# Performance work log

Measured on AMD Instinct MI355X. Metric: run time of the kernel, lower is better.

Reference implementation:

```python
import jax, jax.numpy as jnp
import numpy as np
from jax import lax

DN = ('NDHWC', 'DHWIO', 'NDHWC')
SHAPE = (33, 33, 33)
B = 2
N = 40000
C = 64


def setup_inputs() -> dict:
    key = jax.random.key(0)
    ks = jax.random.split(key, 24)
    D, H, W = SHAPE
    # unique active voxel coords (batch, z, y, x)
    rng = np.random.default_rng(0)
    idx = rng.choice(B * D * H * W, size=N, replace=False)
    b = idx // (D * H * W)
    r = idx % (D * H * W)
    coors = np.stack([b, r // (H * W), (r // W) % H, r % W], axis=1).astype(np.int32)

    def w(k, shape, scale=0.1):
        return jax.random.normal(k, shape, jnp.float32) * scale

    inp = {
        'features': jax.random.normal(ks[0], (N, 3), jnp.float32),
        'coors': jnp.asarray(coors),
        'batch_size': B,
        'w1': w(ks[1], (3, 3, 3, 3, C), 0.2), 'b1': w(ks[2], (C,), 0.05),
        'w2': w(ks[3], (3, 3, 3, C, C), 0.05), 'b2': w(ks[4], (C,), 0.05),
        'w3': w(ks[5], (3, 3, 3, C, C), 0.05), 'b3': w(ks[6], (C,), 0.05),
        'wt': w(ks[7], (3, 3, 3, C, C), 0.05), 'bt': w(ks[8], (C,), 0.05),
        'w5': w(ks[9], (3, 3, 3, C, C), 0.05), 'b5': w(ks[10], (C,), 0.05),
    }
    # folded eval-mode BatchNorm: y = x*s + h  (s = gamma/sqrt(var+eps), h = beta - mean*s)
    for i, (sk, hk) in enumerate(zip(ks[11:16], ks[16:21]), start=1):
        inp[f's{i}'] = 1.0 + 0.1 * jax.random.normal(sk, (C,), jnp.float32)
        inp[f'h{i}'] = 0.05 * jax.random.normal(hk, (C,), jnp.float32)
    return inp


def _forward(features, coors, batch_size,
             w1, b1, w2, b2, w3, b3, wt, bt, w5, b5,
             s1, h1, s2, h2, s3, h3, s4, h4, s5, h5):
    D, H, W = SHAPE
    bi, zi, yi, xi = coors[:, 0], coors[:, 1], coors[:, 2], coors[:, 3]
    # densify SparseConvTensor (zeros at inactive sites) + active mask
    x = jnp.zeros((batch_size, D, H, W, features.shape[-1]), features.dtype)
    x = x.at[bi, zi, yi, xi].set(features)
    m = jnp.zeros((batch_size, D, H, W, 1), jnp.float32).at[bi, zi, yi, xi].set(1.0)
    ones3 = jnp.ones((3, 3, 3, 1, 1), jnp.float32)

    conv = lambda a, k, pad: lax.conv_general_dilated(a, k, (1, 1, 1), pad, dimension_numbers=DN)
    # masked BN(eval) + ReLU: applied only on active sites, background stays exactly 0
    act = lambda y, mm, s, h: jnp.where(mm, jax.nn.relu(y * s + h), 0.0)

    # SparseConv3d(3,64,3): valid conv; output actives = 1-dilation of input actives
    x = conv(x, w1, 'VALID')
    m1 = conv(m, ones3, 'VALID') > 0  # [B,31,31,31,1]
    x = act(x + b1, m1, s1, h1)

    # two SubMConv3d(64,64,3) sharing indice_key: same active set, SAME padding
    x = act(conv(x, w2, 'SAME') + b2, m1, s2, h2)
    x = act(conv(x, w3, 'SAME') + b3, m1, s3, h3)

    # SparseConvTranspose3d(64,64,3,2): out = (D-1)*2+3; actives = transposed dilation
    x = lax.conv_transpose(x, wt, (2, 2, 2), 'VALID', dimension_numbers=DN)
    mT = lax.conv_transpose(m1.astype(jnp.float32), ones3, (2, 2, 2), 'VALID', dimension_numbers=DN) > 0
    x = act(x + bt, mT, s4, h4)

    # ToDense -> dense Conv3d(64,64,3) -> BN -> ReLU (dense: applied everywhere)
    x = conv(x, w5, 'VALID') + b5
    x = jax.nn.relu(x * s5 + h5)
    return jnp.transpose(x, (0, 4, 1, 2, 3))  # NCDHW like spconv ToDense output


def reference(features, coors, batch_size,
              w1, b1, w2, b2, w3, b3, wt, bt, w5, b5,
              s1, h1, s2, h2, s3, h3, s4, h4, s5, h5):
    return _forward(features, coors, batch_size,
                    w1, b1, w2, b2, w3, b3, wt, bt, w5, b5,
                    s1, h1, s2, h2, s3, h3, s4, h4, s5, h5)
```

## Files before the change

### kernel.cpp

```cpp
#include <hip/hip_runtime.h>
#include <cstdint>

constexpr int BB = 2, C = 64;
constexpr int D1 = 31;
constexpr int DP = 33;
constexpr int D4 = 63;
constexpr int D5 = 61;
constexpr int D5CUBE = D5*D5*D5;

constexpr int NV1 = BB*D1*D1*D1;
constexpr int NVP = BB*DP*DP*DP;
constexpr int NV4 = BB*D4*D4*D4;
constexpr int NV5 = BB*D5*D5*D5;

constexpr size_t alup(size_t x) { return (x + 255) & ~(size_t)255; }
constexpr size_t OB_X0  = 0;
constexpr size_t OB_M0  = alup(OB_X0  + (size_t)NVP*3*4);
constexpr size_t OB_M1P = alup(OB_M0  + (size_t)NVP*4);
constexpr size_t OB_X1  = alup(OB_M1P + (size_t)NVP*4);
constexpr size_t OB_X2  = alup(OB_X1  + (size_t)NVP*64*2);
constexpr size_t OB_X3  = alup(OB_X2  + (size_t)NVP*64*2);
constexpr size_t OB_MT  = alup(OB_X3  + (size_t)NVP*64*2);
constexpr size_t OB_X4  = alup(OB_MT  + (size_t)NV4*4);
constexpr size_t OB_WB2 = alup(OB_X4  + (size_t)NV4*64*2);
constexpr size_t OB_WB3 = alup(OB_WB2 + (size_t)27*64*64*2);
constexpr size_t OB_WBT = alup(OB_WB3 + (size_t)27*64*64*2);
constexpr size_t OB_WB5 = alup(OB_WBT + (size_t)27*64*64*2);

typedef __attribute__((ext_vector_type(8))) short short8;
typedef __attribute__((ext_vector_type(4))) float f32x4;

__device__ inline unsigned short f2bf(float f) {
  unsigned int u = __float_as_uint(f);
  u = (u + 0x7FFFu + ((u >> 16) & 1u)) >> 16;
  return (unsigned short)u;
}

template<int DD>
__device__ inline void decodev(int vox, int& b, int& z, int& y, int& x) {
  x = vox % DD; int r = vox / DD;
  y = r % DD;   r /= DD;
  z = r % DD;   b = r / DD;
}

__device__ inline int xcd_swz(int bid, int nb) {
  int q = nb >> 3, r = nb & 7;
  int xcd = bid & 7, idx = bid >> 3;
  return (xcd < r ? xcd*(q+1) : r*(q+1) + (xcd - r)*q) + idx;
}

__global__ void __launch_bounds__(256)
k_zero(float* __restrict__ x0, float* __restrict__ m0, float* __restrict__ m1p,
       unsigned short* __restrict__ x1, unsigned short* __restrict__ x2,
       unsigned short* __restrict__ x3) {
  int v = blockIdx.x*256 + threadIdx.x;
  if (v >= NVP) return;
  m0[v] = 0.f; m1p[v] = 0.f;
  x0[3*v+0] = 0.f; x0[3*v+1] = 0.f; x0[3*v+2] = 0.f;
  int x = v % DP, r = v / DP;
  int y = r % DP; r /= DP;
  int z = r % DP;
  if (x==0 || x==DP-1 || y==0 || y==DP-1 || z==0 || z==DP-1) {
    ulonglong2 zz = {0ull, 0ull};
    ulonglong2* p1 = (ulonglong2*)(x1 + (size_t)v*64);
    ulonglong2* p2 = (ulonglong2*)(x2 + (size_t)v*64);
    ulonglong2* p3 = (ulonglong2*)(x3 + (size_t)v*64);
    #pragma unroll
    for (int i = 0; i < 8; i++) { p1[i] = zz; p2[i] = zz; p3[i] = zz; }
  }
}

__global__ void k_scatter(const float* __restrict__ feat, const int* __restrict__ coors,
                          int n, float* __restrict__ x0, float* __restrict__ m0) {
  int i = blockIdx.x*blockDim.x + threadIdx.x;
  if (i >= n) return;
  int b = coors[4*i+0], z = coors[4*i+1], y = coors[4*i+2], x = coors[4*i+3];
  int v = ((b*DP + z)*DP + y)*DP + x;
  x0[v*3+0] = feat[3*i+0];
  x0[v*3+1] = feat[3*i+1];
  x0[v*3+2] = feat[3*i+2];
  m0[v] = 1.0f;
}

__global__ void __launch_bounds__(256)
k_conv1(const float* __restrict__ x0, const float* __restrict__ m0,
        unsigned short* __restrict__ x1, float* __restrict__ m1p,
        const float* __restrict__ w1, const float* __restrict__ b1,
        const float* __restrict__ s1, const float* __restrict__ h1) {
  long long t = (long long)blockIdx.x*blockDim.x + threadIdx.x;
  if (t >= (long long)NV1*C) return;
  int co  = (int)(t & 63);
  int vox = (int)(t >> 6);
  int b, z, y, x; decodev<D1>(vox, b, z, y, x);
  float sum = 0.f, mm = 0.f;
  #pragma unroll
  for (int kz=0; kz<3; kz++)
  #pragma unroll
  for (int ky=0; ky<3; ky++)
  #pragma unroll
  for (int kx=0; kx<3; kx++) {
    int iv = ((b*DP + z+kz)*DP + y+ky)*DP + (x+kx);
    mm += m0[iv];
    const float* px = x0 + iv*3;
    const float* pw = w1 + ((kz*3+ky)*3+kx)*3*64 + co;
    sum += px[0]*pw[0] + px[1]*pw[64] + px[2]*pw[128];
  }
  bool m = mm > 0.f;
  float o = m ? fmaxf((sum + b1[co])*s1[co] + h1[co], 0.f) : 0.f;
  size_t pOff = (size_t)(((b*DP + z+1)*DP + y+1)*DP + (x+1));
  x1[pOff*C + co] = f2bf(o);
  if (co == 0) m1p[pOff] = m ? 1.f : 0.f;
}

__global__ void k_repack4(const float* __restrict__ wa, const float* __restrict__ wb,
                          const float* __restrict__ wc, const float* __restrict__ wd,
                          unsigned short* __restrict__ da, unsigned short* __restrict__ db,
                          unsigned short* __restrict__ dc, unsigned short* __restrict__ dd) {
  int which = blockIdx.x / 432;
  int i = (blockIdx.x - which*432)*256 + threadIdx.x;
  const float* w = which == 0 ? wa : which == 1 ? wb : which == 2 ? wc : wd;
  unsigned short* dst = which == 0 ? da : which == 1 ? db : which == 2 ? dc : dd;
  int co = i & 63, k = (i >> 6) & 63, t = i >> 12;
  int kk = k >> 5, q = (k >> 3) & 3, j = k & 7, cb = co >> 4, l = q*16 + (co & 15);
  dst[(size_t)((t*2+kk)*4+cb)*512 + l*8 + j] = f2bf(w[i]);
}

template<int NA, int DOUT, int DIN>
__global__ void __launch_bounds__(256)
k_conv_mfma(const unsigned short* __restrict__ inBF, const unsigned short* __restrict__ wB,
            unsigned short* __restrict__ outPtr, const float* __restrict__ m1p,
            const float* __restrict__ bias, const float* __restrict__ s,
            const float* __restrict__ h) {
  constexpr int NVOX = BB*DOUT*DOUT*DOUT;
  const int lane = threadIdx.x & 63;
  const int wid  = threadIdx.x >> 6;
  const int wave = xcd_swz(blockIdx.x, gridDim.x)*4 + wid;
  const int vb   = wave * (NA*16);

  int rowb[NA];
  #pragma unroll
  for (int a = 0; a < NA; a++) {
    int vox = vb + a*16 + (lane & 15);
    vox = vox < NVOX ? vox : NVOX-1;
    int b, z, y, x; decodev<DOUT>(vox, b, z, y, x);
    rowb[a] = (((b*DIN + z)*DIN + y)*DIN + x)*64;
  }
  const int koff = (lane >> 4) * 8;

  f32x4 acc[NA][4];
  #pragma unroll
  for (int a = 0; a < NA; a++)
    #pragma unroll
    for (int cb = 0; cb < 4; cb++)
      acc[a][cb] = f32x4{0.f, 0.f, 0.f, 0.f};

  #pragma unroll 1
  for (int t = 0; t < 27; ++t) {
    int kz = t / 9, rr = t - kz*9;
    int ky = rr / 3, kx = rr - ky*3;
    const int toff = ((kz*DIN + ky)*DIN + kx)*64;
    #pragma unroll
    for (int kk = 0; kk < 2; ++kk) {
      short8 A[NA];
      #pragma unroll
      for (int a = 0; a < NA; a++)
        A[a] = *reinterpret_cast<const short8*>(inBF + rowb[a] + toff + kk*32 + koff);
      short8 Bv[4];
      const unsigned short* wp = wB + (size_t)(t*2+kk)*2048 + lane*8;
      #pragma unroll
      for (int cb = 0; cb < 4; cb++)
        Bv[cb] = *reinterpret_cast<const short8*>(wp + cb*512);
      #pragma unroll
      for (int a = 0; a < NA; a++)
        #pragma unroll
        for (int cb = 0; cb < 4; cb++)
          acc[a][cb] = __builtin_amdgcn_mfma_f32_16x16x32_bf16(A[a], Bv[cb], acc[a][cb], 0, 0, 0);
    }
  }

  float bv[4], sv[4], hv[4];
  #pragma unroll
  for (int cb = 0; cb < 4; cb++) {
    int c = cb*16 + (lane & 15);
    bv[cb] = bias[c]; sv[cb] = s[c]; hv[cb] = h[c];
  }

  #pragma unroll
  for (int a = 0; a < NA; a++)
    #pragma unroll
    for (int r = 0; r < 4; r++) {
      int vox = vb + a*16 + (lane >> 4)*4 + r;
      if (vox >= NVOX) continue;
      int b, z, y, x; decodev<DOUT>(vox, b, z, y, x);
      size_t pOff = (size_t)(((b*DP + z+1)*DP + y+1)*DP + (x+1));
      bool m = m1p[pOff] > 0.f;
      #pragma unroll
      for (int cb = 0; cb < 4; cb++) {
        float o = m ? fmaxf((acc[a][cb][r] + bv[cb])*sv[cb] + hv[cb], 0.f) : 0.f;
        outPtr[pOff*64 + cb*16 + (lane & 15)] = f2bf(o);
      }
    }
}

__global__ void __launch_bounds__(256)
k_maskT(const float* __restrict__ m1p, float* __restrict__ mt) {
  int vox = blockIdx.x*256 + threadIdx.x;
  if (vox >= NV4) return;
  int b, zo, yo, xo; decodev<D4>(vox, b, zo, yo, xo);
  float mm = 0.f;
  for (int kz = 0; kz < 3; kz++) {
    if ((zo + kz) & 1) continue;
    int izp = ((zo + kz - 2) >> 1) + 1;
    for (int ky = 0; ky < 3; ky++) {
      if ((yo + ky) & 1) continue;
      int iyp = ((yo + ky - 2) >> 1) + 1;
      for (int kx = 0; kx < 3; kx++) {
        if ((xo + kx) & 1) continue;
        int ixp = ((xo + kx - 2) >> 1) + 1;
        mm += m1p[((b*DP + izp)*DP + iyp)*DP + ixp];
      }
    }
  }
  mt[vox] = mm;
}

constexpr int CT_CHUNKS = 1792;

__global__ void __launch_bounds__(256)
k_convT_mfma(const unsigned short* __restrict__ x3, const unsigned short* __restrict__ wB,
             unsigned short* __restrict__ x4, const float* __restrict__ mt,
             const float* __restrict__ bias, const float* __restrict__ s,
             const float* __restrict__ h) {
  __shared__ short8 sb[CT_CHUNKS];
  const int tid  = threadIdx.x;
  const int lane = tid & 63;
  const int wid  = tid >> 6;
  const int ii   = lane & 15;
  const int l16  = lane >> 4;

  const int blk   = xcd_swz(blockIdx.x, gridDim.x);
  const int ytile = blk & 15;
  const int rzb   = blk >> 4;
  const int zo    = rzb % D4;
  const int b     = rzb / D4;
  const int y0    = ytile * 4;

  const int izp0 = (zo + (zo & 1)) >> 1;
  const int izp1 = (zo & 1) ? izp0 : izp0 + 1;

  #pragma unroll
  for (int it = 0; it < 7; ++it) {
    int g = it*256 + tid; g = g > 1583 ? 1583 : g;
    int r6 = g / 264, rem = g - r6*264;
    int v = rem >> 3, c16p = rem & 7;
    int c16l = c16p ^ (v & 7);
    int pz  = r6 >= 3 ? 1 : 0;
    int ry  = r6 - pz*3;
    int izp = pz ? izp1 : izp0;
    int iyp = ytile*2 + ry;
    size_t srcB = ((size_t)((b*DP + izp)*DP + iyp)*DP)*128 + (size_t)(v << 7) + (c16l << 4);
    __builtin_amdgcn_global_load_lds(
      (const __attribute__((address_space(1))) void*)((const char*)x3 + srcB),
      (__attribute__((address_space(3))) void*)((char*)&sb[0] + it*4096 + wid*1024),
      16, 0, 0);
  }
  __syncthreads();

  f32x4 acc[4][4];
  #pragma unroll
  for (int a = 0; a < 4; a++)
    #pragma unroll
    for (int cb = 0; cb < 4; cb++)
      acc[a][cb] = f32x4{0.f, 0.f, 0.f, 0.f};

  const int yo = y0 + wid;
  if (yo < D4) {
    const int nPz = (zo & 1) ? 1 : 2;
    #pragma unroll 1
    for (int pz = 0; pz < 2; ++pz) {
      if (pz >= nPz) break;
      const int kz = (zo & 1) ? 1 : pz*2;
      #pragma unroll 1
      for (int kyi = 0; kyi < 2; ++kyi) {
        int ky, ry;
        if (wid & 1) { if (kyi == 1) break; ky = 1; ry = (wid + 1) >> 1; }
        else         { ky = kyi*2;          ry = (wid >> 1) + kyi; }
        const int rbase = (pz*3 + ry)*264;
        #pragma unroll
        for (int kx = 0; kx < 3; ++kx) {
          const int apar  = kx & 1;
          const int xoffE = ((kx + apar - 2) >> 1) + 1;
          const int t = (kz*3 + ky)*3 + kx;
          #pragma unroll
          for (int kk = 0; kk < 2; ++kk) {
            short8 Bv[4];
            const unsigned short* wpk = wB + (size_t)(t*2+kk)*2048 + lane*8;
            #pragma unroll
            for (int cb = 0; cb < 4; cb++)
              Bv[cb] = *reinterpret_cast<const short8*>(wpk + cb*512);
            #pragma unroll
            for (int ablk = 0; ablk < 2; ablk++) {
              const int ixp = ablk*16 + ii + xoffE;
              short8 A = sb[rbase + ixp*8 + ((kk*4 + l16) ^ (ixp & 7))];
              const int afr = apar*2 + ablk;
              #pragma unroll
              for (int cb = 0; cb < 4; cb++)
                acc[afr][cb] = __builtin_amdgcn_mfma_f32_16x16x32_bf16(A, Bv[cb], acc[afr][cb], 0, 0, 0);
            }
          }
        }
      }
    }

    float bv[4], sv[4], hv[4];
    #pragma unroll
    for (int cb = 0; cb < 4; cb++) {
      int c = cb*16 + (lane & 15);
      bv[cb] = bias[c]; sv[cb] = s[c]; hv[cb] = h[c];
    }
    const int rowBase = ((b*D4 + zo)*D4 + yo)*D4;
    #pragma unroll
    for (int a = 0; a < 4; a++) {
      const int ablk = a & 1, apar = a >> 1;
      #pragma unroll
      for (int r = 0; r < 4; r++) {
        const int row = (lane >> 4)*4 + r;
        const int xo  = 2*(ablk*16 + row) + apar;
        if (xo >= D4) continue;
        const int vox = rowBase + xo;
        const bool m = mt[vox] > 0.f;
        #pragma unroll
        for (int cb = 0; cb < 4; cb++) {
          float o = m ? fmaxf((acc[a][cb][r] + bv[cb])*sv[cb] + hv[cb], 0.f) : 0.f;
          x4[(size_t)vox*64 + cb*16 + (lane & 15)] = f2bf(o);
        }
      }
    }
  }
}

__device__ __forceinline__ void c5_step(const short8 (&A)[4], const short8 (&W)[4],
                                        f32x4 (&acc)[4][4]) {
  #pragma unroll
  for (int a = 0; a < 4; a++)
    #pragma unroll
    for (int cb = 0; cb < 4; cb++)
      acc[a][cb] = __builtin_amdgcn_mfma_f32_16x16x32_bf16(W[cb], A[a], acc[a][cb], 0, 0, 0);
}

__global__ void __launch_bounds__(256, 2)
k_conv5_mfma(const unsigned short* __restrict__ x4, const unsigned short* __restrict__ wB,
             float* __restrict__ out, const float* __restrict__ bias,
             const float* __restrict__ s, const float* __restrict__ h) {
  __shared__ short8 sA[2][2048];
  const int tid  = threadIdx.x;
  const int lane = tid & 63;
  const int wid  = tid >> 6;
  const int ll   = lane & 15;
  const int l16  = lane >> 4;

  const int blk   = xcd_swz(blockIdx.x, gridDim.x);
  const int ytile = blk & 15;
  const int rzb   = blk >> 4;
  const int z     = rzb % D5;
  const int b     = rzb / D5;
  const int y0    = ytile * 4;

  int st_r[8], st_base[8];
  #pragma unroll
  for (int it = 0; it < 8; ++it) {
    int g = it*256 + tid; g = g > 2015 ? 2015 : g;
    int r = g / 504, rem = g - r*504;
    int v = rem >> 3, c16p = rem & 7;
    int c16l = c16p ^ (v & 7);
    st_r[it] = r;
    st_base[it] = (v << 7) + (c16l << 4);
  }

  const char* x4b = (const char*)x4;

  f32x4 acc[4][4];
  #pragma unroll
  for (int a = 0; a < 4; a++)
    #pragma unroll
    for (int cb = 0; cb < 4; cb++)
      acc[a][cb] = f32x4{0.f, 0.f, 0.f, 0.f};

  auto STAGE_A = [&](int kzn, int kyn, int hn) {
    size_t pb = (size_t)(b*D4 + z + kzn) * (D4*D4*128);
    char* dst = (char*)&sA[hn][0];
    #pragma unroll
    for (int it = 0; it < 8; ++it) {
      int yin = y0 + st_r[it] + kyn; yin = yin > 62 ? 62 : yin;
      __builtin_amdgcn_global_load_lds(
        (const __attribute__((address_space(1))) void*)(x4b + pb + (size_t)yin*8064 + st_base[it]),
        (__attribute__((address_space(3))) void*)(dst + it*4096 + wid*1024),
        16, 0, 0);
    }
  };
  auto LDA = [&](int hh, int kx, int kk, short8 (&A)[4]) {
    #pragma unroll
    for (int a = 0; a < 4; a++) {
      int v  = a*16 + ll + kx;
      int ch = wid*504 + v*8 + ((kk*4 + l16) ^ (v & 7));
      A[a] = sA[hh][ch];
    }
  };

  short8 A0[4], A1[4], A2[4];

  STAGE_A(0, 0, 0);
  __syncthreads();

#define C5_BODY(p0,p1,p2,p3,p4,p5)                                    \
  do {                                                                 \
    LDA(hh, (p0)>>1, (p0)&1, A0);                                      \
    LDA(hh, (p1)>>1, (p1)&1, A1);                                      \
    LDA(hh, (p2)>>1, (p2)&1, A2);  c5_step(A0, W[p0], acc);            \
    LDA(hh, (p3)>>1, (p3)&1, A0);  c5_step(A1, W[p1], acc);            \
    LDA(hh, (p4)>>1, (p4)&1, A1);  c5_step(A2, W[p2], acc);            \
    LDA(hh, (p5)>>1, (p5)&1, A2);  c5_step(A0, W[p3], acc);            \
    c5_step(A1, W[p4], acc);                                           \
    c5_step(A2, W[p5], acc);                                           \
  } while (0)

  int kzn = 0, kyn = 1;
  #pragma unroll 1
  for (int p = 0; p < 9; ++p) {
    const int hh = p & 1;

    short8 W[6][4];
    {
      const unsigned short* wp = wB + (size_t)p*12288 + lane*8;
      #pragma unroll
      for (int st = 0; st < 6; ++st)
        #pragma unroll
        for (int cb = 0; cb < 4; cb++)
          W[st][cb] = *reinterpret_cast<const short8*>(wp + st*2048 + cb*512);
    }
    __builtin_amdgcn_sched_barrier(0);

    if (p < 8) {
      STAGE_A(kzn, kyn, hh ^ 1);
      kyn++; if (kyn == 3) { kyn = 0; kzn++; }
    }
    __builtin_amdgcn_sched_barrier(0);

    if ((wid & 1) == 0) {
      C5_BODY(0,1,2,3,4,5);
    } else {
      C5_BODY(3,4,5,0,1,2);
    }
    __syncthreads();
  }
#undef C5_BODY

  const int yout = y0 + wid;
  if (yout < D5) {
    #pragma unroll
    for (int a = 0; a < 4; a++) {
      int x = a*16 + ll;
      if (x >= D5) continue;
      size_t sp = (size_t)(z*D5 + yout)*D5 + x;
      #pragma unroll
      for (int cb = 0; cb < 4; cb++)
        #pragma unroll
        for (int r = 0; r < 4; r++) {
          int co = cb*16 + l16*4 + r;
          float o = fmaxf((acc[a][cb][r] + bias[co])*s[co] + h[co], 0.f);
          out[(size_t)(b*64 + co)*D5CUBE + sp] = o;
        }
    }
  }
}

extern "C" void kernel_launch(void* const* d_in, const int* in_sizes, int n_in,
                              void* d_out, int out_size, void* d_ws, size_t ws_size,
                              hipStream_t stream) {
  const float* feat  = (const float*)d_in[0];
  const int*   coors = (const int*)d_in[1];
  const float* w1 = (const float*)d_in[3];
  const float* b1 = (const float*)d_in[4];
  const float* w2 = (const float*)d_in[5];
  const float* b2 = (const float*)d_in[6];
  const float* w3 = (const float*)d_in[7];
  const float* b3 = (const float*)d_in[8];
  const float* wt = (const float*)d_in[9];
  const float* bt = (const float*)d_in[10];
  const float* w5 = (const float*)d_in[11];
  const float* b5 = (const float*)d_in[12];
  const float* s1 = (const float*)d_in[13];
  const float* h1 = (const float*)d_in[14];
  const float* s2 = (const float*)d_in[15];
  const float* h2 = (const float*)d_in[16];
  const float* s3 = (const float*)d_in[17];
  const float* h3 = (const float*)d_in[18];
  const float* s4 = (const float*)d_in[19];
  const float* h4 = (const float*)d_in[20];
  const float* s5 = (const float*)d_in[21];
  const float* h5 = (const float*)d_in[22];
  int n = in_sizes[0] / 3;

  char* wsb = (char*)d_ws;
  float*          X0  = (float*)(wsb + OB_X0);
  float*          M0  = (float*)(wsb + OB_M0);
  float*          M1P = (float*)(wsb + OB_M1P);
  unsigned short* X1  = (unsigned short*)(wsb + OB_X1);
  unsigned short* X2  = (unsigned short*)(wsb + OB_X2);
  unsigned short* X3  = (unsigned short*)(wsb + OB_X3);
  float*          MT  = (float*)(wsb + OB_MT);
  unsigned short* X4  = (unsigned short*)(wsb + OB_X4);
  unsigned short* WB2 = (unsigned short*)(wsb + OB_WB2);
  unsigned short* WB3 = (unsigned short*)(wsb + OB_WB3);
  unsigned short* WBT = (unsigned short*)(wsb + OB_WBT);
  unsigned short* WB5 = (unsigned short*)(wsb + OB_WB5);

  k_zero<<<(NVP + 255)/256, 256, 0, stream>>>(X0, M0, M1P, X1, X2, X3);

  k_repack4<<<1728, 256, 0, stream>>>(w2, w3, wt, w5, WB2, WB3, WBT, WB5);

  k_scatter<<<(n+255)/256, 256, 0, stream>>>(feat, coors, n, X0, M0);

  {
    long long threads = (long long)NV1*C;
    k_conv1<<<(int)((threads+255)/256), 256, 0, stream>>>(X0, M0, X1, M1P, w1, b1, s1, h1);
  }

  constexpr int WAVES23 = (NV1 + 31) / 32;
  constexpr int BLK23   = (WAVES23 + 3) / 4;
  k_conv_mfma<2, D1, DP><<<BLK23, 256, 0, stream>>>(X1, WB2, X2, M1P, b2, s2, h2);
  k_conv_mfma<2, D1, DP><<<BLK23, 256, 0, stream>>>(X2, WB3, X3, M1P, b3, s3, h3);

  k_maskT<<<(NV4 + 255)/256, 256, 0, stream>>>(M1P, MT);

  constexpr int BLK_T = BB * D4 * 16;
  k_convT_mfma<<<BLK_T, 256, 0, stream>>>(X3, WBT, X4, MT, bt, s4, h4);

  constexpr int BLK5 = BB * D5 * 16;
  k_conv5_mfma<<<BLK5, 256, 0, stream>>>(X4, WB5, (float*)d_out, b5, s5, h5);
}
```

Baseline: 349.3 us.

## Stage conv2/3 input rows in LDS and split conv5 x-tiles

Replaces the per-voxel global-load conv2/conv3 kernel with a row-tiled kernel that stages input rows into double-buffered LDS via global_load_lds and reuses them across kx taps, and packs bf16 outputs into 64-bit stores. Conv5 is re-tiled so each block handles half the x range with smaller accumulators and LDS, doubling the block count and dropping the min-occupancy launch bound. The intent is to cut redundant global loads in conv2/3 and raise occupancy and parallelism in conv5, at the cost of weights being reloaded per block twice as often in conv5.

```diff
diff --git a/kernel.cpp b/kernel.cpp
--- a/kernel.cpp
+++ b/kernel.cpp
@@ -123,83 +123,6 @@
   int co = i & 63, k = (i >> 6) & 63, t = i >> 12;
   int kk = k >> 5, q = (k >> 3) & 3, j = k & 7, cb = co >> 4, l = q*16 + (co & 15);
   dst[(size_t)((t*2+kk)*4+cb)*512 + l*8 + j] = f2bf(w[i]);
-}
-
-template<int NA, int DOUT, int DIN>
-__global__ void __launch_bounds__(256)
-k_conv_mfma(const unsigned short* __restrict__ inBF, const unsigned short* __restrict__ wB,
-            unsigned short* __restrict__ outPtr, const float* __restrict__ m1p,
-            const float* __restrict__ bias, const float* __restrict__ s,
-            const float* __restrict__ h) {
-  constexpr int NVOX = BB*DOUT*DOUT*DOUT;
-  const int lane = threadIdx.x & 63;
-  const int wid  = threadIdx.x >> 6;
-  const int wave = xcd_swz(blockIdx.x, gridDim.x)*4 + wid;
-  const int vb   = wave * (NA*16);
-
-  int rowb[NA];
-  #pragma unroll
-  for (int a = 0; a < NA; a++) {
-    int vox = vb + a*16 + (lane & 15);
-    vox = vox < NVOX ? vox : NVOX-1;
-    int b, z, y, x; decodev<DOUT>(vox, b, z, y, x);
-    rowb[a] = (((b*DIN + z)*DIN + y)*DIN + x)*64;
-  }
-  const int koff = (lane >> 4) * 8;
-
-  f32x4 acc[NA][4];
-  #pragma unroll
-  for (int a = 0; a < NA; a++)
-    #pragma unroll
-    for (int cb = 0; cb < 4; cb++)
-      acc[a][cb] = f32x4{0.f, 0.f, 0.f, 0.f};
-
-  #pragma unroll 1
-  for (int t = 0; t < 27; ++t) {
-    int kz = t / 9, rr = t - kz*9;
-    int ky = rr / 3, kx = rr - ky*3;
-    const int toff = ((kz*DIN + ky)*DIN + kx)*64;
-    #pragma unroll
-    for (int kk = 0; kk < 2; ++kk) {
-      short8 A[NA];
-      #pragma unroll
-      for (int a = 0; a < NA; a++)
-        A[a] = *reinterpret_cast<const short8*>(inBF + rowb[a] + toff + kk*32 + koff);
-      short8 Bv[4];
-      const unsigned short* wp = wB + (size_t)(t*2+kk)*2048 + lane*8;
-      #pragma unroll
-      for (int cb = 0; cb < 4; cb++)
-        Bv[cb] = *reinterpret_cast<const short8*>(wp + cb*512);
-      #pragma unroll
-      for (int a = 0; a < NA; a++)
-        #pragma unroll
-        for (int cb = 0; cb < 4; cb++)
-          acc[a][cb] = __builtin_amdgcn_mfma_f32_16x16x32_bf16(A[a], Bv[cb], acc[a][cb], 0, 0, 0);
-    }
-  }
-
-  float bv[4], sv[4], hv[4];
-  #pragma unroll
-  for (int cb = 0; cb < 4; cb++) {
-    int c = cb*16 + (lane & 15);
-    bv[cb] = bias[c]; sv[cb] = s[c]; hv[cb] = h[c];
-  }
-
-  #pragma unroll
-  for (int a = 0; a < NA; a++)
-    #pragma unroll
-    for (int r = 0; r < 4; r++) {
-      int vox = vb + a*16 + (lane >> 4)*4 + r;
-      if (vox >= NVOX) continue;
-      int b, z, y, x; decodev<DOUT>(vox, b, z, y, x);
-      size_t pOff = (size_t)(((b*DP + z+1)*DP + y+1)*DP + (x+1));
-      bool m = m1p[pOff] > 0.f;
-      #pragma unroll
-      for (int cb = 0; cb < 4; cb++) {
-        float o = m ? fmaxf((acc[a][cb][r] + bv[cb])*sv[cb] + hv[cb], 0.f) : 0.f;
-        outPtr[pOff*64 + cb*16 + (lane & 15)] = f2bf(o);
-      }
-    }
 }
 
 __global__ void __launch_bounds__(256)
@@ -222,6 +145,140 @@
     }
   }
   mt[vox] = mm;
+}
+
+__device__ __forceinline__ void c_step2(const short8 (&A)[2], const short8 (&W)[4],
+                                        f32x4 (&acc)[2][4]) {
+  #pragma unroll
+  for (int a = 0; a < 2; a++)
+    #pragma unroll
+    for (int cb = 0; cb < 4; cb++)
+      acc[a][cb] = __builtin_amdgcn_mfma_f32_16x16x32_bf16(W[cb], A[a], acc[a][cb], 0, 0, 0);
+}
+
+constexpr int C23_HALF = 1280;
+
+__global__ void __launch_bounds__(256)
+k_conv23_mfma(const unsigned short* __restrict__ xin, const unsigned short* __restrict__ wB,
+              unsigned short* __restrict__ xout, const float* __restrict__ m1p,
+              const float* __restrict__ bias, const float* __restrict__ s,
+              const float* __restrict__ h) {
+  __shared__ short8 sA[2*C23_HALF];
+  const int tid  = threadIdx.x;
+  const int lane = tid & 63;
+  const int wid  = tid >> 6;
+  const int ll   = lane & 15;
+  const int l16  = lane >> 4;
+
+  const int blk = xcd_swz(blockIdx.x, gridDim.x);
+  const int yt  = blk & 7;
+  const int rzb = blk >> 3;
+  const int z   = rzb % D1;
+  const int b   = rzb / D1;
+  const int y0  = yt * 4;
+
+  int st_r[5], st_base[5];
+  #pragma unroll
+  for (int it = 0; it < 5; ++it) {
+    int g = it*256 + tid; g = g > 1055 ? 1055 : g;
+    int r = g / 264, rem = g - r*264;
+    int v = rem >> 3, c16p = rem & 7;
+    int c16l = c16p ^ (v & 7);
+    st_r[it] = r;
+    st_base[it] = (v << 7) + (c16l << 4);
+  }
+
+  const char* xinb = (const char*)xin;
+
+  f32x4 acc[2][4];
+  #pragma unroll
+  for (int a = 0; a < 2; a++)
+    #pragma unroll
+    for (int cb = 0; cb < 4; cb++)
+      acc[a][cb] = f32x4{0.f, 0.f, 0.f, 0.f};
+
+  auto STAGE = [&](int kzn, int kyn, int hn) {
+    size_t pb = (size_t)((b*DP + z + kzn)*DP) * (DP*128);
+    char* dst = (char*)&sA[0] + hn*(C23_HALF*16);
+    #pragma unroll
+    for (int it = 0; it < 5; ++it) {
+      int yin = y0 + st_r[it] + kyn; yin = yin > 32 ? 32 : yin;
+      __builtin_amdgcn_global_load_lds(
+        (const __attribute__((address_space(1))) void*)(xinb + pb + (size_t)yin*(DP*128) + st_base[it]),
+        (__attribute__((address_space(3))) void*)(dst + it*4096 + wid*1024),
+        16, 0, 0);
+    }
+  };
+  auto LDA = [&](int hh, int kx, int kk, short8 (&A)[2]) {
+    #pragma unroll
+    for (int a = 0; a < 2; a++) {
+      int xv = a*16 + ll; xv = xv > 30 ? 30 : xv;
+      int v  = xv + kx;
+      int ch = hh*C23_HALF + wid*264 + v*8 + ((kk*4 + l16) ^ (v & 7));
+      A[a] = sA[ch];
+    }
+  };
+
+  short8 A0[2], A1[2];
+
+  STAGE(0, 0, 0);
+  __syncthreads();
+
+  int kzn = 0, kyn = 1;
+  #pragma unroll 1
+  for (int p = 0; p < 9; ++p) {
+    const int hh = p & 1;
+
+    short8 W[6][4];
+    {
+      const unsigned short* wp = wB + (size_t)p*12288 + lane*8;
+      #pragma unroll
+      for (int st = 0; st < 6; ++st)
+        #pragma unroll
+        for (int cb = 0; cb < 4; cb++)
+          W[st][cb] = *reinterpret_cast<const short8*>(wp + st*2048 + cb*512);
+    }
+    __builtin_amdgcn_sched_barrier(0);
+
+    if (p < 8) {
+      STAGE(kzn, kyn, hh ^ 1);
+      kyn++; if (kyn == 3) { kyn = 0; kzn++; }
+    }
+    __builtin_amdgcn_sched_barrier(0);
+
+    LDA(hh, 0, 0, A0);
+    #pragma unroll
+    for (int st = 0; st < 6; ++st) {
+      const int kxn = (st+1) >> 1, kkn = (st+1) & 1;
+      if (st < 5) {
+        if (st & 1) LDA(hh, kxn, kkn, A0); else LDA(hh, kxn, kkn, A1);
+      }
+      if (st & 1) c_step2(A1, W[st], acc); else c_step2(A0, W[st], acc);
+    }
+    __syncthreads();
+  }
+
+  const int y = y0 + wid;
+  if (y < D1) {
+    #pragma unroll
+    for (int a = 0; a < 2; a++) {
+      int x = a*16 + ll;
+      if (x >= D1) continue;
+      size_t pOff = (size_t)(((b*DP + z+1)*DP + y+1)*DP + (x+1));
+      bool m = m1p[pOff] > 0.f;
+      #pragma unroll
+      for (int cb = 0; cb < 4; cb++) {
+        unsigned long long pack = 0;
+        #pragma unroll
+        for (int r = 0; r < 4; r++) {
+          int co = cb*16 + l16*4 + r;
+          float o = m ? fmaxf((acc[a][cb][r] + bias[co])*s[co] + h[co], 0.f) : 0.f;
+          pack |= (unsigned long long)f2bf(o) << (16*r);
+        }
+        *reinterpret_cast<unsigned long long*>(xout + pOff*64 + cb*16 + l16*4) = pack;
+      }
+    }
+  }
 }
 
 constexpr int CT_CHUNKS = 1792;
@@ -339,90 +396,69 @@
   }
 }
 
-__device__ __forceinline__ void c5_step(const short8 (&A)[4], const short8 (&W)[4],
-                                        f32x4 (&acc)[4][4]) {
-  #pragma unroll
-  for (int a = 0; a < 4; a++)
-    #pragma unroll
-    for (int cb = 0; cb < 4; cb++)
-      acc[a][cb] = __builtin_amdgcn_mfma_f32_16x16x32_bf16(W[cb], A[a], acc[a][cb], 0, 0, 0);
-}
-
-__global__ void __launch_bounds__(256, 2)
+__global__ void __launch_bounds__(256)
 k_conv5_mfma(const unsigned short* __restrict__ x4, const unsigned short* __restrict__ wB,
              float* __restrict__ out, const float* __restrict__ bias,
              const float* __restrict__ s, const float* __restrict__ h) {
-  __shared__ short8 sA[2][2048];
+  __shared__ short8 sA[2][1280];
   const int tid  = threadIdx.x;
   const int lane = tid & 63;
   const int wid  = tid >> 6;
   const int ll   = lane & 15;
   const int l16  = lane >> 4;
 
-  const int blk   = xcd_swz(blockIdx.x, gridDim.x);
-  const int ytile = blk & 15;
-  const int rzb   = blk >> 4;
-  const int z     = rzb % D5;
-  const int b     = rzb / D5;
-  const int y0    = ytile * 4;
-
-  int st_r[8], st_base[8];
-  #pragma unroll
-  for (int it = 0; it < 8; ++it) {
-    int g = it*256 + tid; g = g > 2015 ? 2015 : g;
-    int r = g / 504, rem = g - r*504;
-    int v = rem >> 3, c16p = rem & 7;
+  const int blk = xcd_swz(blockIdx.x, gridDim.x);
+  const int xt  = blk & 1;
+  const int yt  = (blk >> 1) & 15;
+  const int rzb = blk >> 5;
+  const int z   = rzb % D5;
+  const int b   = rzb / D5;
+  const int y0  = yt * 4;
+  const int xbase = xt * 32;
+
+  int st_off[5];
+  #pragma unroll
+  for (int it = 0; it < 5; ++it) {
+    int g = it*64 + lane;
+    int v = g >> 3, c16p = g & 7;
     int c16l = c16p ^ (v & 7);
-    st_r[it] = r;
-    st_base[it] = (v << 7) + (c16l << 4);
+    st_off[it] = xt*4096 + (v << 7) + (c16l << 4);
   }
 
   const char* x4b = (const char*)x4;
 
-  f32x4 acc[4][4];
-  #pragma unroll
-  for (int a = 0; a < 4; a++)
+  f32x4 acc[2][4];
+  #pragma unroll
+  for (int a = 0; a < 2; a++)
     #pragma unroll
     for (int cb = 0; cb < 4; cb++)
       acc[a][cb] = f32x4{0.f, 0.f, 0.f, 0.f};
 
-  auto STAGE_A = [&](int kzn, int kyn, int hn) {
-    size_t pb = (size_t)(b*D4 + z + kzn) * (D4*D4*128);
-    char* dst = (char*)&sA[hn][0];
-    #pragma unroll
-    for (int it = 0; it < 8; ++it) {
-      int yin = y0 + st_r[it] + kyn; yin = yin > 62 ? 62 : yin;
+  auto STAGE = [&](int kzn, int kyn, int hn) {
+    int yin = y0 + wid + kyn; yin = yin > 62 ? 62 : yin;
+    size_t rb = ((size_t)((b*D4 + z + kzn)*D4 + yin)) * 8064;
+    char* dst = (char*)&sA[hn][0] + wid*5120;
+    #pragma unroll
+    for (int it = 0; it < 5; ++it) {
       __builtin_amdgcn_global_load_lds(
-        (const __attribute__((address_space(1))) void*)(x4b + pb + (size_t)yin*8064 + st_base[it]),
-        (__attribute__((address_space(3))) void*)(dst + it*4096 + wid*1024),
+        (const __attribute__((address_space(1))) void*)(x4b + rb + st_off[it]),
+        (__attribute__((address_space(3))) void*)(dst + it*1024),
         16, 0, 0);
     }
   };
-  auto LDA = [&](int hh, int kx, int kk, short8 (&A)[4]) {
-    #pragma unroll
-    for (int a = 0; a < 4; a++) {
-      int v  = a*16 + ll + kx;
-      int ch = wid*504 + v*8 + ((kk*4 + l16) ^ (v & 7));
-      A[a] = sA[hh][ch];
+  auto LDA = [&](int hh, int kx, int kk, short8 (&A)[2]) {
+    #pragma unroll
+    for (int a = 0; a < 2; a++) {
+      int v = a*16 + ll + kx;
+      int ch = hh*1280 + wid*320 + v*8 + ((kk*4 + l16) ^ (v & 7));
+      A[a] = sA[0][ch];
     }
   };
 
-  short8 A0[4], A1[4], A2[4];
-
-  STAGE_A(0, 0, 0);
+  short8 A0[2], A1[2];
+
+  STAGE(0, 0, 0);
   __syncthreads();
-
-#define C5_BODY(p0,p1,p2,p3,p4,p5)                                    \
-  do {                                                                 \
-    LDA(hh, (p0)>>1, (p0)&1, A0);                                      \
-    LDA(hh, (p1)>>1, (p1)&1, A1);                                      \
-    LDA(hh, (p2)>>1, (p2)&1, A2);  c5_step(A0, W[p0], acc);            \
-    LDA(hh, (p3)>>1, (p3)&1, A0);  c5_step(A1, W[p1], acc);            \
-    LDA(hh, (p4)>>1, (p4)&1, A1);  c5_step(A2, W[p2], acc);            \
-    LDA(hh, (p5)>>1, (p5)&1, A2);  c5_step(A0, W[p3], acc);            \
-    c5_step(A1, W[p4], acc);                                           \
-    c5_step(A2, W[p5], acc);                                           \
-  } while (0)
 
   int kzn = 0, kyn = 1;
   #pragma unroll 1
@@ -441,25 +477,28 @@
     __builtin_amdgcn_sched_barrier(0);
 
     if (p < 8) {
-      STAGE_A(kzn, kyn, hh ^ 1);
+      STAGE(kzn, kyn, hh ^ 1);
       kyn++; if (kyn == 3) { kyn = 0; kzn++; }
     }
     __builtin_amdgcn_sched_barrier(0);
 
-    if ((wid & 1) == 0) {
-      C5_BODY(0,1,2,3,4,5);
-    } else {
-      C5_BODY(3,4,5,0,1,2);
+    LDA(hh, 0, 0, A0);
+    #pragma unroll
+    for (int st = 0; st < 6; ++st) {
+      const int kxn = (st+1) >> 1, kkn = (st+1) & 1;
+      if (st < 5) {
+        if (st & 1) LDA(hh, kxn, kkn, A0); else LDA(hh, kxn, kkn, A1);
+      }
+      if (st & 1) c_step2(A1, W[st], acc); else c_step2(A0, W[st], acc);
     }
     __syncthreads();
   }
-#undef C5_BODY
 
   const int yout = y0 + wid;
   if (yout < D5) {
     #pragma unroll
-    for (int a = 0; a < 4; a++) {
-      int x = a*16 + ll;
+    for (int a = 0; a < 2; a++) {
+      int x = xbase + a*16 + ll;
       if (x >= D5) continue;
       size_t sp = (size_t)(z*D5 + yout)*D5 + x;
       #pragma unroll
@@ -526,16 +565,15 @@
     k_conv1<<<(int)((threads+255)/256), 256, 0, stream>>>(X0, M0, X1, M1P, w1, b1, s1, h1);
   }
 
-  constexpr int WAVES23 = (NV1 + 31) / 32;
-  constexpr int BLK23   = (WAVES23 + 3) / 4;
-  k_conv_mfma<2, D1, DP><<<BLK23, 256, 0, stream>>>(X1, WB2, X2, M1P, b2, s2, h2);
-  k_conv_mfma<2, D1, DP><<<BLK23, 256, 0, stream>>>(X2, WB3, X3, M1P, b3, s3, h3);
+  constexpr int BLK23 = BB * D1 * 8;
+  k_conv23_mfma<<<BLK23, 256, 0, stream>>>(X1, WB2, X2, M1P, b2, s2, h2);
+  k_conv23_mfma<<<BLK23, 256, 0, stream>>>(X2, WB3, X3, M1P, b3, s3, h3);
 
   k_maskT<<<(NV4 + 255)/256, 256, 0, stream>>>(M1P, MT);
 
   constexpr int BLK_T = BB * D4 * 16;
   k_convT_mfma<<<BLK_T, 256, 0, stream>>>(X3, WBT, X4, MT, bt, s4, h4);
 
-  constexpr int BLK5 = BB * D5 * 16;
+  constexpr int BLK5 = BB * D5 * 16 * 2;
   k_conv5_mfma<<<BLK5, 256, 0, stream>>>(X4, WB5, (float*)d_out, b5, s5, h5);
 }
```

Measured after the change: 355.9 us. No clear change (+1.9%).
